# Kernel optimization log

Hardware: AMD Instinct MI355X
Metric: run time of the kernel (lower is better)

The kernel has to match this reference:

```python
import jax, jax.numpy as jnp
import numpy as np

B, L, D = 2, 2048, 2048
H, HKV, HD = 16, 4, 128
GROUPS = H // HKV


def _rope_tables(key):
    # standard RoPE cos/sin tables, shape (B, L, HD)
    inv_freq = 1.0 / (10000.0 ** (jnp.arange(0, HD, 2, dtype=jnp.float32) / HD))
    pos = jnp.arange(L, dtype=jnp.float32)
    freqs = pos[:, None] * inv_freq[None, :]          # (L, HD/2)
    emb = jnp.concatenate([freqs, freqs], axis=-1)    # (L, HD)
    cos = jnp.broadcast_to(jnp.cos(emb)[None], (B, L, HD))
    sin = jnp.broadcast_to(jnp.sin(emb)[None], (B, L, HD))
    return cos, sin


def setup_inputs() -> dict:
    key = jax.random.key(0)
    ks = jax.random.split(key, 5)
    x = jax.random.normal(ks[0], (B, L, D), dtype=jnp.float32)
    cos, sin = _rope_tables(ks[1])
    s = 1.0 / np.sqrt(D)
    Wq = jax.random.normal(ks[2], (D, D), dtype=jnp.float32) * s
    bq = jnp.zeros((D,), dtype=jnp.float32)
    Wkv = jax.random.normal(ks[3], (2 * HKV * HD, D), dtype=jnp.float32) * s
    bkv = jnp.zeros((2 * HKV * HD,), dtype=jnp.float32)
    Wo = jax.random.normal(ks[4], (D, D), dtype=jnp.float32) * s
    bo = jnp.zeros((D,), dtype=jnp.float32)
    return {"x": x, "cos": cos, "sin": sin, "Wq": Wq, "bq": bq,
            "Wkv": Wkv, "bkv": bkv, "Wo": Wo, "bo": bo}


def _rotate_half(t):
    t1, t2 = jnp.split(t, 2, axis=-1)
    return jnp.concatenate([-t2, t1], axis=-1)


def reference(x, cos, sin, Wq, bq, Wkv, bkv, Wo, bo):
    b, l, d = x.shape
    # QKV projections
    q = (x @ Wq.T + bq).reshape(b, l, H, HD)
    kv = (x @ Wkv.T + bkv).reshape(b, l, 2, HKV, HD)
    k, v = kv[:, :, 0], kv[:, :, 1]
    # RoPE (unsqueeze over head dim, layout B,L,H,D)
    c = cos[:, :, None, :]
    s = sin[:, :, None, :]
    q = q * c + _rotate_half(q) * s
    k = k * c + _rotate_half(k) * s
    # GQA: expand kv heads to query heads
    k = jnp.repeat(k, GROUPS, axis=2)
    v = jnp.repeat(v, GROUPS, axis=2)
    # causal attention (flash_attn_func equivalent math)
    scores = jnp.einsum("blhd,bmhd->bhlm", q, k) / jnp.sqrt(jnp.float32(HD))
    mask = jnp.tril(jnp.ones((l, l), dtype=bool))
    scores = jnp.where(mask[None, None], scores, jnp.finfo(scores.dtype).min)
    attn = jax.nn.softmax(scores, axis=-1)
    out = jnp.einsum("bhlm,bmhd->blhd", attn, v).reshape(b, l, H * HD)
    return out @ Wo.T + bo
```

## Files before the change

### kernel.cpp

```cpp
#include <hip/hip_runtime.h>
#include <hip/hip_bf16.h>
#include <cstddef>

constexpr int B = 2, L = 2048, D = 2048;
constexpr int H = 16, HKV = 4, HD = 128;
constexpr int GROUPS = H / HKV;
constexpr int KVD = 2 * HKV * HD;
constexpr int M_ROWS = B * L;
constexpr int QKVW = D + KVD;

typedef __attribute__((ext_vector_type(8))) short short8;
typedef __attribute__((ext_vector_type(4))) short s16x4;
typedef __attribute__((ext_vector_type(4))) float f32x4;

__device__ __forceinline__ short f2bf(float f) {
    union { float f; unsigned u; } v; v.f = f;
    unsigned r = v.u + 0x7FFFu + ((v.u >> 16) & 1u);
    return (short)(r >> 16);
}

__device__ __forceinline__ float fast_exp2(float x) {
#if __has_builtin(__builtin_amdgcn_exp2f)
    return __builtin_amdgcn_exp2f(x);
#else
    return exp2f(x);
#endif
}

__device__ __forceinline__ int invp(int pos) {
    const int b16 = pos >> 4, j = pos & 15;
    return ((b16 >> 1) << 4) + j + ((b16 & 1) << 6);
}

typedef __attribute__((address_space(1))) const void cg_void;
typedef __attribute__((address_space(3))) void lds_void;
__device__ __forceinline__ void gl_lds16(const void* g, void* l) {
    __builtin_amdgcn_global_load_lds((cg_void*)g, (lds_void*)l, 16, 0, 0);
}

__global__ __launch_bounds__(256) void cast_all(
    const float* __restrict__ x, const float* __restrict__ Wq,
    const float* __restrict__ Wkv, const float* __restrict__ Wo,
    const float* __restrict__ bq, const float* __restrict__ bkv,
    short* __restrict__ xb, short* __restrict__ wqkvb, short* __restrict__ wob,
    float* __restrict__ bqkv)
{
    constexpr int n_x   = M_ROWS * D / 4;
    constexpr int n_wq  = D * D / 4;
    constexpr int n_wkv = KVD * D / 4;
    constexpr int n_wo  = D * D / 4;
    constexpr int n_w   = n_x + n_wq + n_wkv + n_wo;
    constexpr int RPW   = D / 4;
    int i = blockIdx.x * 256 + threadIdx.x;
    if (i >= n_w) {
        const int j = i - n_w;
        float4 o;
#pragma unroll
        for (int e = 0; e < 4; ++e) {
            const int idx = j * 4 + e;
            float v;
            if (idx < D)                 v = bq[((idx >> 7) << 7) + invp(idx & 127)];
            else if (idx < D + HKV * HD) v = bkv[(((idx - D) >> 7) << 7) + invp((idx - D) & 127)];
            else                         v = bkv[idx - D];
            (&o.x)[e] = v;
        }
        ((float4*)bqkv)[j] = o;
        return;
    }
    const float* src; short* dst; int isrc;
    if (i < n_x) {
        src = x; dst = xb; isrc = i;
    } else if (i < n_x + n_wq) {
        i -= n_x; src = Wq; dst = wqkvb;
        const int fi = i / RPW, col = i % RPW;
        const int head = fi >> 7, pos = fi & 127;
        isrc = ((head << 7) + invp(pos)) * RPW + col;
    } else if (i < n_x + n_wq + n_wkv) {
        i -= n_x + n_wq; src = Wkv; dst = wqkvb + (size_t)D * D;
        const int fi = i / RPW, col = i % RPW;
        if (fi < HKV * HD) {
            isrc = (((fi >> 7) << 7) + invp(fi & 127)) * RPW + col;
        } else {
            isrc = i;
        }
    } else {
        i -= n_x + n_wq + n_wkv; src = Wo; dst = wob; isrc = i;
    }
    const float4 f = ((const float4*)src)[isrc];
    s16x4 s;
    s[0] = f2bf(f.x); s[1] = f2bf(f.y); s[2] = f2bf(f.z); s[3] = f2bf(f.w);
    ((s16x4*)dst)[i] = s;
}

template<int MODE>
__global__ __launch_bounds__(512, 2) void gemm256(
    const short* __restrict__ Ag, const short* __restrict__ Wg,
    const float* __restrict__ bias, float* __restrict__ C,
    const float* __restrict__ cosp, const float* __restrict__ sinp,
    short* __restrict__ qout, short* __restrict__ kout, short* __restrict__ vtout,
    int M, int N, int K)
{
    __shared__ __align__(1024) char smem[131072];

    const int tid = threadIdx.x;
    const int w = tid >> 6, lane = tid & 63;
    const int quad = lane >> 4, n16 = lane & 15;
    const int wr = w >> 2, wc = w & 3;

    const int nbx = gridDim.x;
    const int nwg = nbx * gridDim.y;
    int wg = blockIdx.y * nbx + blockIdx.x;
    wg = (wg & 7) * (nwg >> 3) + (wg >> 3);
    const int bm = (wg / nbx) << 8;
    const int bn = (wg % nbx) << 8;

    const int nkt = K >> 6;

    const int sbo = n16 * 64 + ((quad * 16) ^ ((n16 & 8) << 2));

    const int srow = lane >> 2;
    const int scol = ((lane & 3) * 8) ^ (((lane >> 5) & 1) << 4);

    f32x4 acc[8][4];
#pragma unroll
    for (int i = 0; i < 8; ++i)
#pragma unroll
        for (int j = 0; j < 4; ++j)
#pragma unroll
            for (int r = 0; r < 4; ++r) acc[i][j][r] = 0.f;

    short8 afr[4][2], bfr[4][2];

#define STAGE_A(k0, cb, h)                                                     \
    { _Pragma("unroll") for (int j = 0; j < 2; ++j) {                          \
        const int s  = w + j * 8;                                              \
        const int u  = s >> 1;                                                 \
        const int rg = ((u >> 2) << 3) + ((h) << 2) + (u & 3);                 \
        const int gr = bm + (rg << 4) + srow;                                  \
        const int gc = (k0) + ((s & 1) << 5) + scol;                           \
        gl_lds16(Ag + (size_t)gr * K + gc,                                     \
                 smem + (cb) * 32768 + (h) * 16384 + (s << 10)); } }

#define STAGE_B(k0, cb, h)                                                     \
    { _Pragma("unroll") for (int j = 0; j < 2; ++j) {                          \
        const int s  = w + j * 8;                                              \
        const int u  = s >> 1;                                                 \
        const int rg = ((u >> 1) << 2) + ((h) << 1) + (u & 1);                 \
        const int gr = bn + (rg << 4) + srow;                                  \
        const int gc = (k0) + ((s & 1) << 5) + scol;                           \
        gl_lds16(Wg + (size_t)gr * K + gc,                                     \
                 smem + 65536 + (cb) * 32768 + (h) * 16384 + (s << 10)); } }

#define PHASE(CB, MH, RDB, STAGE_STMT, WAIT_STMT)                              \
    {                                                                          \
        if (RDB) {                                                             \
            _Pragma("unroll") for (int nj = 0; nj < 4; ++nj)                   \
            _Pragma("unroll") for (int kk = 0; kk < 2; ++kk)                   \
                bfr[nj][kk] = *(const short8*)(smem + 65536 + (CB) * 32768 +   \
                    (nj >> 1) * 16384 +                                        \
                    ((((wc * 2 + (nj & 1)) * 2) + kk) << 10) + sbo);           \
        }                                                                      \
        _Pragma("unroll") for (int mi2 = 0; mi2 < 4; ++mi2)                    \
        _Pragma("unroll") for (int kk = 0; kk < 2; ++kk)                       \
            afr[mi2][kk] = *(const short8*)(smem + (CB) * 32768 +              \
                (MH) * 16384 + ((((wr * 4 + mi2) * 2) + kk) << 10) + sbo);     \
        STAGE_STMT;                                                            \
        WAIT_STMT;                                                             \
        __builtin_amdgcn_s_barrier();                                          \
        asm volatile("s_waitcnt lgkmcnt(0)" ::: "memory");                     \
        __builtin_amdgcn_sched_barrier(0);                                     \
        __builtin_amdgcn_s_setprio(1);                                         \
        _Pragma("unroll") for (int mi2 = 0; mi2 < 4; ++mi2)                    \
        _Pragma("unroll") for (int nj = 0; nj < 4; ++nj)                       \
        _Pragma("unroll") for (int kk = 0; kk < 2; ++kk)                       \
            acc[(MH) * 4 + mi2][nj] =                                          \
                __builtin_amdgcn_mfma_f32_16x16x32_bf16(                       \
                    afr[mi2][kk], bfr[nj][kk], acc[(MH) * 4 + mi2][nj],        \
                    0, 0, 0);                                                  \
        __builtin_amdgcn_s_setprio(0);                                         \
        asm volatile("" ::: "memory");                                         \
        __builtin_amdgcn_s_barrier();                                          \
    }

#define NOP_WAIT asm volatile("" ::: "memory")

    STAGE_A(0, 0, 0);
    STAGE_B(0, 0, 0);
    STAGE_A(0, 0, 1);
    STAGE_B(0, 0, 1);
    if (nkt > 1) {
        STAGE_A(64, 1, 0);
        STAGE_B(64, 1, 0);
        asm volatile("s_waitcnt vmcnt(4)" ::: "memory");
    } else {
        asm volatile("s_waitcnt vmcnt(0)" ::: "memory");
    }
    __builtin_amdgcn_s_barrier();

    for (int t = 0; t < nkt; t += 2) {
        const int k1 = (t + 1) << 6, k2 = (t + 2) << 6, k3 = (t + 3) << 6;
        const bool g2 = (t + 2) < nkt, g3 = (t + 3) < nkt;

        PHASE(0, 0, 1, { STAGE_A(k1, 1, 1); STAGE_B(k1, 1, 1); }, NOP_WAIT);
        PHASE(0, 1, 0, { if (g2) { STAGE_A(k2, 0, 0); STAGE_B(k2, 0, 0); } },
              { if (g2) asm volatile("s_waitcnt vmcnt(4)" ::: "memory");
                else    asm volatile("s_waitcnt vmcnt(0)" ::: "memory"); });

        PHASE(1, 0, 1, { if (g2) { STAGE_A(k2, 0, 1); STAGE_B(k2, 0, 1); } }, NOP_WAIT);
        PHASE(1, 1, 0, { if (g3) { STAGE_A(k3, 1, 0); STAGE_B(k3, 1, 0); } },
              { if (g3) asm volatile("s_waitcnt vmcnt(4)" ::: "memory");
                else    asm volatile("s_waitcnt vmcnt(0)" ::: "memory"); });
    }

#undef PHASE
#undef STAGE_A
#undef STAGE_B
#undef NOP_WAIT

    if (MODE == 0) {
#pragma unroll
        for (int mh = 0; mh < 2; ++mh)
#pragma unroll
            for (int mi2 = 0; mi2 < 4; ++mi2)
#pragma unroll
                for (int r = 0; r < 4; ++r) {
                    const int row = bm + wr * 128 + mh * 64 + mi2 * 16 + quad * 4 + r;
#pragma unroll
                    for (int nh = 0; nh < 2; ++nh)
#pragma unroll
                        for (int ni2 = 0; ni2 < 2; ++ni2) {
                            const int col = bn + wc * 64 + nh * 32 + ni2 * 16 + n16;
                            C[(size_t)row * N + col] =
                                acc[mh * 4 + mi2][nh * 2 + ni2][r] + bias[col];
                        }
                }
    } else {
        short* const T = (short*)smem;
        __syncthreads();
        if (bn < D + HKV * HD) {
#pragma unroll
            for (int mh = 0; mh < 2; ++mh)
#pragma unroll
                for (int mi2 = 0; mi2 < 4; ++mi2)
#pragma unroll
                    for (int r = 0; r < 4; ++r) {
                        const int rl = wr * 128 + mh * 64 + mi2 * 16 + quad * 4 + r;
                        const int row = bm + rl;
                        const float* csrow = cosp + (size_t)row * HD;
                        const float* snrow = sinp + (size_t)row * HD;
                        const int sw = ((rl >> 2) & 7) << 4;
#pragma unroll
                        for (int nh = 0; nh < 2; ++nh) {
                            const int cl = wc * 64 + nh * 32 + n16;
                            const int iif = (wc & 1) * 32 + nh * 16 + n16;
                            const float a  = acc[mh * 4 + mi2][nh * 2 + 0][r] + bias[bn + cl];
                            const float bb = acc[mh * 4 + mi2][nh * 2 + 1][r] + bias[bn + cl + 16];
                            const float olo = a * csrow[iif]       - bb * snrow[iif];
                            const float ohi = bb * csrow[iif + 64] + a * snrow[iif + 64];
                            *(short*)((char*)T + ((rl * 512 + cl * 2) ^ sw))        = f2bf(olo);
                            *(short*)((char*)T + ((rl * 512 + (cl + 16) * 2) ^ sw)) = f2bf(ohi);
                        }
                    }
            __syncthreads();
            const bool isK = (bn >= D);
#pragma unroll
            for (int it = 0; it < 16; ++it) {
                const int idx = it * 512 + tid;
                const int rl = idx >> 5, c8 = idx & 31;
                const short8 v = *(const short8*)((char*)T +
                    ((rl * 512 + c8 * 16) ^ (((rl >> 2) & 7) << 4)));
                const int row = bm + rl;
                if (!isK) {
                    *(short8*)&qout[(size_t)row * D + bn + c8 * 8] = v;
                } else {
                    const int ck = bn - D + c8 * 8;
                    const int hk = ck >> 7, dk = ck & 127;
                    const int b_ = row >> 11, l_ = row & (L - 1);
                    *(short8*)&kout[((size_t)(b_ * HKV + hk) * L + l_) * HD + dk] = v;
                }
            }
        } else {
#pragma unroll
            for (int mh = 0; mh < 2; ++mh)
#pragma unroll
                for (int mi2 = 0; mi2 < 4; ++mi2) {
                    const int l0 = wr * 128 + mh * 64 + mi2 * 16 + quad * 4;
#pragma unroll
                    for (int nh = 0; nh < 2; ++nh)
#pragma unroll
                        for (int ni2 = 0; ni2 < 2; ++ni2) {
                            const int cl = wc * 64 + nh * 32 + ni2 * 16 + n16;
                            const float bs = bias[bn + cl];
                            s16x4 sv;
#pragma unroll
                            for (int r = 0; r < 4; ++r)
                                sv[r] = f2bf(acc[mh * 4 + mi2][nh * 2 + ni2][r] + bs);
                            *(s16x4*)((char*)T + ((cl * 512 + l0 * 2) ^ ((cl & 7) << 4))) = sv;
                        }
                }
            __syncthreads();
#pragma unroll
            for (int it = 0; it < 16; ++it) {
                const int idx = it * 512 + tid;
                const int cvr = idx >> 5, l8 = idx & 31;
                const short8 v = *(const short8*)((char*)T +
                    ((cvr * 512 + l8 * 16) ^ ((cvr & 7) << 4)));
                const int cv = bn - (D + HKV * HD) + cvr;
                const int hv = cv >> 7, dv = cv & 127;
                const int b_ = bm >> 11;
                const int lg = (bm & (L - 1)) + l8 * 8;
                *(short8*)&vtout[((size_t)(b_ * HKV + hv) * HD + dv) * L + lg] = v;
            }
        }
    }
}

__global__ __launch_bounds__(512) void attn_mfma4(
    const short* __restrict__ qb_, const short* __restrict__ kb_,
    const short* __restrict__ vtb_, short* __restrict__ ob)
{
    __shared__ __align__(16) char smem[86016];
    short* const KsB  = (short*)smem;
    short* const VtB  = (short*)(smem + 32768);
    short* const PbB  = (short*)(smem + 65536);
    float* const Rbuf = (float*)smem;

    const int hkv = blockIdx.y, b = blockIdx.z;
    const int tid = threadIdx.x;
    const int w = tid >> 6, lane = tid & 63;
    const int quad = lane >> 4, n16 = lane & 15;
    const int h   = hkv * GROUPS + (w & 3);
    const int kh  = (w >> 2) * 32;
    const int khg = (w >> 2) * 4;

    const size_t kbase  = (size_t)(b * HKV + hkv) * L * HD;
    const size_t vtbase = (size_t)(b * HKV + hkv) * HD * L;
    const float c1 = 0.12751845f;
    const float c0 = -28.853901f;

    short8 ones;
#pragma unroll
    for (int i = 0; i < 8; ++i) ones[i] = (short)0x3F80;

    const int kr = lane >> 4;
    const int kg_sw = lane & 15;
    const int vr = lane >> 3;
    const int vg_sw = lane & 7;

    short* const myPb = PbB + w * (2 * 16 * 40);

#pragma unroll 1
    for (int phase = 0; phase < 2; ++phase) {
        const int qidx = phase ? (63 - (int)blockIdx.x) : (int)blockIdx.x;
        const int qb0 = qidx * 32;
        const int ntiles = (qidx >> 1) + 1;

        short8 qf[2][4];
#pragma unroll
        for (int rt = 0; rt < 2; ++rt)
#pragma unroll
            for (int kk = 0; kk < 4; ++kk)
                qf[rt][kk] = *(const short8*)&qb_[
                    ((size_t)(b * L + qb0 + rt * 16 + n16)) * D + h * HD + kk * 32 + quad * 8];

        f32x4 oacc[2][8], lacc[2];
#pragma unroll
        for (int rt = 0; rt < 2; ++rt) {
#pragma unroll
            for (int r = 0; r < 4; ++r) lacc[rt][r] = 0.f;
#pragma unroll
            for (int nt = 0; nt < 8; ++nt)
#pragma unroll
                for (int r = 0; r < 4; ++r) oacc[rt][nt][r] = 0.f;
        }

        __syncthreads();

        {
            const short* kg = kb_ + kbase;
            const short* vg = vtb_ + vtbase;
#pragma unroll
            for (int j = 0; j < 2; ++j) {
                const int chunk = w * 2 + j;
                const int r = chunk * 4 + kr;
                gl_lds16(kg + r * HD + (kg_sw ^ (r & 15)) * 8, KsB + chunk * 512);
            }
#pragma unroll
            for (int j = 0; j < 2; ++j) {
                const int chunk = w * 2 + j;
                const int d = chunk * 8 + vr;
                gl_lds16(vg + (size_t)d * L + (vg_sw ^ (d & 7)) * 8, VtB + chunk * 512);
            }
        }

        for (int kt = 0; kt < ntiles; ++kt) {
            const int buf = kt & 1;
            __syncthreads();

            if (kt + 1 < ntiles) {
                const short* kg = kb_ + kbase + (size_t)((kt + 1) * 64) * HD;
                const short* vg = vtb_ + vtbase + (kt + 1) * 64;
#pragma unroll
                for (int j = 0; j < 2; ++j) {
                    const int chunk = w * 2 + j;
                    const int r = chunk * 4 + kr;
                    gl_lds16(kg + r * HD + (kg_sw ^ (r & 15)) * 8,
                             KsB + (buf ^ 1) * 8192 + chunk * 512);
                }
#pragma unroll
                for (int j = 0; j < 2; ++j) {
                    const int chunk = w * 2 + j;
                    const int d = chunk * 8 + vr;
                    gl_lds16(vg + (size_t)d * L + (vg_sw ^ (d & 7)) * 8,
                             VtB + (buf ^ 1) * 8192 + chunk * 512);
                }
            }

            const short* Ks = KsB + buf * 8192;
            const short* Vt = VtB + buf * 8192;

            f32x4 s[2][2];
#pragma unroll
            for (int rt = 0; rt < 2; ++rt)
#pragma unroll
                for (int ktl = 0; ktl < 2; ++ktl)
#pragma unroll
                    for (int r = 0; r < 4; ++r) s[rt][ktl][r] = 0.f;
#pragma unroll
            for (int kk = 0; kk < 4; ++kk) {
                short8 kf[2];
#pragma unroll
                for (int ktl = 0; ktl < 2; ++ktl) {
                    const int row = kh + ktl * 16 + n16;
                    kf[ktl] = *(const short8*)&Ks[row * 128 + ((kk * 4 + quad) ^ n16) * 8];
                }
#pragma unroll
                for (int rt = 0; rt < 2; ++rt)
#pragma unroll
                    for (int ktl = 0; ktl < 2; ++ktl)
                        s[rt][ktl] = __builtin_amdgcn_mfma_f32_16x16x32_bf16(
                            qf[rt][kk], kf[ktl], s[rt][ktl], 0, 0, 0);
            }

            const bool lastt = (kt == ntiles - 1);
#pragma unroll
            for (int rt = 0; rt < 2; ++rt) {
#pragma unroll
                for (int ktl = 0; ktl < 2; ++ktl) {
                    const int key0 = kt * 64 + kh + ktl * 16 + n16;
#pragma unroll
                    for (int r = 0; r < 4; ++r) {
                        float sv = s[rt][ktl][r];
                        if (lastt) {
                            const int qi = qb0 + rt * 16 + quad * 4 + r;
                            sv = (key0 <= qi) ? sv : -1e30f;
                        }
                        const float e = fast_exp2(sv * c1 + c0);
                        myPb[(rt * 16 + quad * 4 + r) * 40 + ktl * 16 + n16] = f2bf(e);
                    }
                }
            }
            asm volatile("s_waitcnt lgkmcnt(0)" ::: "memory");

            short8 pf[2];
#pragma unroll
            for (int rt = 0; rt < 2; ++rt)
                pf[rt] = *(const short8*)&myPb[(rt * 16 + n16) * 40 + quad * 8];
#pragma unroll
            for (int rt = 0; rt < 2; ++rt)
                lacc[rt] = __builtin_amdgcn_mfma_f32_16x16x32_bf16(pf[rt], ones, lacc[rt], 0, 0, 0);
#pragma unroll
            for (int nt = 0; nt < 8; ++nt) {
                const short8 vf = *(const short8*)&Vt[
                    (nt * 16 + n16) * 64 + ((khg + quad) ^ (n16 & 7)) * 8];
#pragma unroll
                for (int rt = 0; rt < 2; ++rt)
                    oacc[rt][nt] = __builtin_amdgcn_mfma_f32_16x16x32_bf16(pf[rt], vf, oacc[rt][nt], 0, 0, 0);
            }
        }

        __syncthreads();
        if (w >= 4) {
            float* rp = Rbuf + ((size_t)(w - 4) * 64 + lane) * 76;
#pragma unroll
            for (int rt = 0; rt < 2; ++rt)
#pragma unroll
                for (int nt = 0; nt < 8; ++nt)
                    *(f32x4*)&rp[(rt * 8 + nt) * 4] = oacc[rt][nt];
            *(f32x4*)&rp[64] = lacc[0];
            *(f32x4*)&rp[68] = lacc[1];
        }
        __syncthreads();
        if (w < 4) {
            const float* rp = Rbuf + ((size_t)w * 64 + lane) * 76;
#pragma unroll
            for (int rt = 0; rt < 2; ++rt) {
                const f32x4 lr = *(const f32x4*)&rp[64 + rt * 4];
#pragma unroll
                for (int r = 0; r < 4; ++r) lacc[rt][r] += lr[r];
#pragma unroll
                for (int nt = 0; nt < 8; ++nt) {
                    const f32x4 o2 = *(const f32x4*)&rp[(rt * 8 + nt) * 4];
#pragma unroll
                    for (int r = 0; r < 4; ++r) oacc[rt][nt][r] += o2[r];
                }
            }
#pragma unroll
            for (int rt = 0; rt < 2; ++rt) {
#pragma unroll
                for (int r = 0; r < 4; ++r) {
                    const float inv = 1.0f / lacc[rt][r];
                    short* op = ob + ((size_t)(b * L + qb0 + rt * 16 + quad * 4 + r)) * D + h * HD + n16;
#pragma unroll
                    for (int nt = 0; nt < 8; ++nt) op[nt * 16] = f2bf(oacc[rt][nt][r] * inv);
                }
            }
        }
    }
}

extern "C" void kernel_launch(void* const* d_in, const int* in_sizes, int n_in,
                              void* d_out, int out_size, void* d_ws, size_t ws_size,
                              hipStream_t stream)
{
    const float* x    = (const float*)d_in[0];
    const float* cosp = (const float*)d_in[1];
    const float* sinp = (const float*)d_in[2];
    const float* Wq   = (const float*)d_in[3];
    const float* bq   = (const float*)d_in[4];
    const float* Wkv  = (const float*)d_in[5];
    const float* bkv  = (const float*)d_in[6];
    const float* Wo   = (const float*)d_in[7];
    const float* bo   = (const float*)d_in[8];
    float* out = (float*)d_out;

    char* p = (char*)d_ws;
    short* x_bf    = (short*)p; p += (size_t)M_ROWS * D * 2;
    short* wqkv_bf = (short*)p; p += (size_t)QKVW * D * 2;
    short* wo_bf   = (short*)p; p += (size_t)D * D * 2;
    float* b_qkv   = (float*)p; p += (size_t)QKVW * 4;
    short* q_bf    = (short*)p; p += (size_t)M_ROWS * D * 2;
    short* k_bf    = (short*)p; p += (size_t)M_ROWS * HKV * HD * 2;
    short* vt_bf   = (short*)p;
    short* attn_bf = x_bf;

    dim3 blk(256);

    cast_all<<<dim3(18435), blk, 0, stream>>>(
        x, Wq, Wkv, Wo, bq, bkv, x_bf, wqkv_bf, wo_bf, b_qkv);

    gemm256<1><<<dim3(QKVW / 256, M_ROWS / 256), dim3(512), 0, stream>>>(
        x_bf, wqkv_bf, b_qkv, nullptr, cosp, sinp, q_bf, k_bf, vt_bf,
        M_ROWS, QKVW, D);

    attn_mfma4<<<dim3(32, HKV, B), dim3(512), 0, stream>>>(q_bf, k_bf, vt_bf, attn_bf);

    gemm256<0><<<dim3(D / 256, M_ROWS / 256), dim3(512), 0, stream>>>(
        attn_bf, wo_bf, bo, out, nullptr, nullptr, nullptr, nullptr, nullptr,
        M_ROWS, D, D);
}
```

Measured before the change: 298.3 us.

## Add dedicated 128x256-tile output projection GEMM with double-buffered LDS pipeline

Replaces the generic 256x256 gemm256 for the output projection with a new gemm_out kernel using 128x256 tiles, giving twice as many workgroups (256 instead of 128) to fill the device's compute units. It uses double-buffered LDS staging via direct global-to-LDS loads, split-K-half phases with barriers, a swizzled workgroup remapping for L2 locality, and occupancy hint of 2 blocks per CU. The cost is lower arithmetic intensity per tile and a duplicated specialised GEMM kernel.

```diff
diff --git a/kernel.cpp b/kernel.cpp
--- a/kernel.cpp
+++ b/kernel.cpp
@@ -315,6 +315,126 @@
     }
 }
 
+__global__ __launch_bounds__(512, 2) void gemm_out(
+    const short* __restrict__ Ag, const short* __restrict__ Wg,
+    const float* __restrict__ bias, float* __restrict__ C,
+    int M, int N, int K)
+{
+    __shared__ __align__(1024) char smem[98304];
+
+    const int tid = threadIdx.x;
+    const int w = tid >> 6, lane = tid & 63;
+    const int quad = lane >> 4, n16 = lane & 15;
+    const int wr = w >> 2, wc = w & 3;
+
+    const int nbx = gridDim.x;
+    const int nwg = nbx * gridDim.y;
+    int wg = blockIdx.y * nbx + blockIdx.x;
+    wg = (wg & 7) * (nwg >> 3) + (wg >> 3);
+    const int bm = (wg / nbx) << 7;
+    const int bn = (wg % nbx) << 8;
+
+    const int nkt = K >> 6;
+
+    const int sbo = n16 * 64 + ((quad * 16) ^ ((n16 & 8) << 2));
+    const int srow = lane >> 2;
+    const int scol = ((lane & 3) * 8) ^ (((lane >> 5) & 1) << 4);
+
+    f32x4 acc[4][4];
+#pragma unroll
+    for (int i = 0; i < 4; ++i)
+#pragma unroll
+        for (int j = 0; j < 4; ++j)
+#pragma unroll
+            for (int r = 0; r < 4; ++r) acc[i][j][r] = 0.f;
+
+    short8 afr[4], bfr[4];
+
+#define OSTAGE_A(k0, cb, kh)                                                   \
+    { const int gr = bm + (w << 4) + srow;                                     \
+      const int gc = (k0) + ((kh) << 5) + scol;                                \
+      gl_lds16(Ag + (size_t)gr * K + gc,                                       \
+               smem + (cb) * 16384 + (kh) * 8192 + (w << 10)); }
+
+#define OSTAGE_B(k0, cb, kh)                                                   \
+    { _Pragma("unroll") for (int j = 0; j < 2; ++j) {                          \
+        const int s = w + j * 8;                                               \
+        const int gr = bn + (s << 4) + srow;                                   \
+        const int gc = (k0) + ((kh) << 5) + scol;                              \
+        gl_lds16(Wg + (size_t)gr * K + gc,                                     \
+                 smem + 32768 + (cb) * 32768 + (kh) * 16384 + (s << 10)); } }
+
+#define OPHASE(CB, KH, STAGE_STMT, WAIT_STMT)                                  \
+    {                                                                          \
+        _Pragma("unroll") for (int mi = 0; mi < 4; ++mi)                       \
+            afr[mi] = *(const short8*)(smem + (CB) * 16384 + (KH) * 8192 +     \
+                ((wr * 4 + mi) << 10) + sbo);                                  \
+        _Pragma("unroll") for (int nj = 0; nj < 4; ++nj)                       \
+            bfr[nj] = *(const short8*)(smem + 32768 + (CB) * 32768 +           \
+                (KH) * 16384 + ((wc * 4 + nj) << 10) + sbo);                   \
+        STAGE_STMT;                                                            \
+        WAIT_STMT;                                                             \
+        __builtin_amdgcn_s_barrier();                                          \
+        asm volatile("s_waitcnt lgkmcnt(0)" ::: "memory");                     \
+        __builtin_amdgcn_sched_barrier(0);                                     \
+        __builtin_amdgcn_s_setprio(1);                                         \
+        _Pragma("unroll") for (int mi = 0; mi < 4; ++mi)                       \
+        _Pragma("unroll") for (int nj = 0; nj < 4; ++nj)                       \
+            acc[mi][nj] = __builtin_amdgcn_mfma_f32_16x16x32_bf16(             \
+                afr[mi], bfr[nj], acc[mi][nj], 0, 0, 0);                       \
+        __builtin_amdgcn_s_setprio(0);                                         \
+        asm volatile("" ::: "memory");                                         \
+        __builtin_amdgcn_s_barrier();                                          \
+    }
+
+#define ONOP asm volatile("" ::: "memory")
+
+    OSTAGE_A(0, 0, 0);
+    OSTAGE_B(0, 0, 0);
+    OSTAGE_A(0, 0, 1);
+    OSTAGE_B(0, 0, 1);
+    if (nkt > 1) {
+        OSTAGE_A(64, 1, 0);
+        OSTAGE_B(64, 1, 0);
+        asm volatile("s_waitcnt vmcnt(3)" ::: "memory");
+    } else {
+        asm volatile("s_waitcnt vmcnt(0)" ::: "memory");
+    }
+    __builtin_amdgcn_s_barrier();
+
+    for (int t = 0; t < nkt; t += 2) {
+        const int k1 = (t + 1) << 6, k2 = (t + 2) << 6, k3 = (t + 3) << 6;
+        const bool g2 = (t + 2) < nkt, g3 = (t + 3) < nkt;
+
+        OPHASE(0, 0, { OSTAGE_A(k1, 1, 1); OSTAGE_B(k1, 1, 1); }, ONOP);
+        OPHASE(0, 1, { if (g2) { OSTAGE_A(k2, 0, 0); OSTAGE_B(k2, 0, 0); } },
+               { if (g2) asm volatile("s_waitcnt vmcnt(3)" ::: "memory");
+                 else    asm volatile("s_waitcnt vmcnt(0)" ::: "memory"); });
+
+        OPHASE(1, 0, { if (g2) { OSTAGE_A(k2, 0, 1); OSTAGE_B(k2, 0, 1); } }, ONOP);
+        OPHASE(1, 1, { if (g3) { OSTAGE_A(k3, 1, 0); OSTAGE_B(k3, 1, 0); } },
+               { if (g3) asm volatile("s_waitcnt vmcnt(3)" ::: "memory");
+                 else    asm volatile("s_waitcnt vmcnt(0)" ::: "memory"); });
+    }
+
+#undef OPHASE
+#undef OSTAGE_A
+#undef OSTAGE_B
+#undef ONOP
+
+#pragma unroll
+    for (int mi = 0; mi < 4; ++mi)
+#pragma unroll
+        for (int r = 0; r < 4; ++r) {
+            const int row = bm + wr * 64 + mi * 16 + quad * 4 + r;
+#pragma unroll
+            for (int nj = 0; nj < 4; ++nj) {
+                const int col = bn + wc * 64 + nj * 16 + n16;
+                C[(size_t)row * N + col] = acc[mi][nj][r] + bias[col];
+            }
+        }
+}
+
 __global__ __launch_bounds__(512) void attn_mfma4(
     const short* __restrict__ qb_, const short* __restrict__ kb_,
     const short* __restrict__ vtb_, short* __restrict__ ob)
@@ -555,7 +675,6 @@
 
     attn_mfma4<<<dim3(32, HKV, B), dim3(512), 0, stream>>>(q_bf, k_bf, vt_bf, attn_bf);
 
-    gemm256<0><<<dim3(D / 256, M_ROWS / 256), dim3(512), 0, stream>>>(
-        attn_bf, wo_bf, bo, out, nullptr, nullptr, nullptr, nullptr, nullptr,
-        M_ROWS, D, D);
-}
+    gemm_out<<<dim3(D / 256, M_ROWS / 128), dim3(512), 0, stream>>>(
+        attn_bf, wo_bf, bo, out, M_ROWS, D, D);
+}
```

Measured after the change: 281.7 us. -5.6%, faster.
